# Kernel tuning notes

Hardware: AMD Instinct MI355X
Metric: run time of the kernel (lower is better)

## Reference

```python
import jax, jax.numpy as jnp
import numpy as np
from jax import lax

THRESH = 0.1  # stand-in for os.environ['THRESHOLD']
DN = ('NCHW', 'OIHW', 'NCHW')


def _prelu(x, a):
    # nn.PReLU() with a single shared parameter a (init 0.25)
    return jnp.where(x >= 0, x, a[0] * x)


def _nan_conv(x, w, b):
    # NaNConv2d: skip (zero out) input activations with |x| < THRESH,
    # then a standard 3x3 conv, stride 1, padding 1.
    xm = jnp.where(jnp.abs(x) >= THRESH, x, jnp.zeros((), x.dtype))
    y = lax.conv_general_dilated(xm, w, window_strides=(1, 1),
                                 padding='SAME', dimension_numbers=DN)
    return y + b[None, :, None, None]


def setup_inputs() -> dict:
    key = jax.random.key(0)
    ks = jax.random.split(key, 8)
    B, C, H, W = 8, 256, 128, 128
    x = jax.random.normal(ks[0], (B, C, H, W), dtype=jnp.float32)
    w_scale = 0.05  # keep activations numerically tame
    w1 = jax.random.normal(ks[1], (C, C, 3, 3), dtype=jnp.float32) * w_scale
    b1 = jax.random.normal(ks[2], (C,), dtype=jnp.float32) * w_scale
    w2 = jax.random.normal(ks[3], (C, C, 3, 3), dtype=jnp.float32) * w_scale
    b2 = jax.random.normal(ks[4], (C,), dtype=jnp.float32) * w_scale
    w3 = jax.random.normal(ks[5], (C, C, 3, 3), dtype=jnp.float32) * w_scale
    b3 = jax.random.normal(ks[6], (C,), dtype=jnp.float32) * w_scale
    prelu_a = jnp.full((1,), 0.25, dtype=jnp.float32)  # nn.PReLU default init
    return {'x': x, 'w1': w1, 'b1': b1, 'w2': w2, 'b2': b2,
            'w3': w3, 'b3': b3, 'prelu_a': prelu_a}


def reference(x, w1, b1, w2, b2, w3, b3, prelu_a):
    # x0 = NaNConv(prelu(x))
    x0 = _nan_conv(_prelu(x, prelu_a), w1, b1)
    # cat+max over trailing dim == elementwise max
    x1_max = jnp.maximum(x, x0)
    x1 = _prelu(x1_max, prelu_a)
    x1c = _nan_conv(x1, w2, b2)
    x2_max = jnp.maximum(x1c, x1_max)
    x2 = _prelu(x2_max, prelu_a)
    out = _nan_conv(x2, w3, b3)
    return out
```

## Files before the change

### kernel.cpp

```cpp
#include <hip/hip_runtime.h>
#include <cstddef>

#define THRESH 0.1f

constexpr int Bn = 8, C = 256, H = 128, W = 128;
constexpr int HW = H * W;
constexpr size_t CHW = (size_t)C * HW;
constexpr int WSZ = 9 * 256 * 256;
constexpr int WT_ELEM = 18432;
constexpr int ACT_ELEM = 4 * 132 * 32;
constexpr int SA_BYTES = (WT_ELEM + ACT_ELEM) * 2;

typedef __attribute__((ext_vector_type(8))) short short8;
typedef __attribute__((ext_vector_type(4))) float f32x4;

__device__ __forceinline__ float bf2f(ushort u) {
    union { unsigned u; float f; } v; v.u = ((unsigned)u) << 16; return v.f;
}
__device__ __forceinline__ ushort f2bf(float f) {
    union { float f; unsigned u; } v; v.f = f;
    unsigned r = v.u + 0x7FFF + ((v.u >> 16) & 1);
    return (ushort)(r >> 16);
}
__device__ __forceinline__ float pm(float x, float a) {
    float t = (x >= 0.f) ? x : a * x;
    return (fabsf(t) >= THRESH) ? t : 0.f;
}

__device__ __forceinline__ void load_lds16(const void* g, void* l) {
    __builtin_amdgcn_global_load_lds(
        (const __attribute__((address_space(1))) unsigned int*)g,
        (__attribute__((address_space(3))) unsigned int*)l, 16, 0, 0);
}

__global__ void wtrans_kernel(const float* __restrict__ w1,
                              const float* __restrict__ w2,
                              const float* __restrict__ w3,
                              ushort* __restrict__ Wtf)
{
    const float* src = (blockIdx.z == 0) ? w1 : (blockIdx.z == 1) ? w2 : w3;
    ushort* dst = Wtf + (size_t)blockIdx.z * WSZ;
    int idx = blockIdx.x * 256 + threadIdx.x;
    int co = idx >> 8, ci = idx & 255;
    int cb  = co >> 6;
    int m   = (co >> 4) & 3;
    int l15 = co & 15;
    int cib = ci >> 5;
    int l4  = (ci >> 3) & 3;
    int j   = ci & 7;
    int lane = l15 + 16 * l4;
    for (int t = 0; t < 9; ++t) {
        float v = src[((size_t)co * 256 + ci) * 9 + t];
        size_t o = ((((size_t)cb * 8 + cib) * 9 + t) * 4 + m) * 512 + lane * 8 + j;
        dst[o] = f2bf(v);
    }
}

__global__ __launch_bounds__(256) void xt1_kernel(const float* __restrict__ x,
                                                  const float* __restrict__ pa,
                                                  ushort* __restrict__ Xt)
{
    __shared__ float sl[64][133];
    int tid = threadIdx.x;
    int ci0 = blockIdx.x * 64, h = blockIdx.y, b = blockIdx.z;
    float a = pa[0];
    int wcol = tid & 127, chalf = tid >> 7;
    const float* xb = x + (size_t)b * CHW + (size_t)ci0 * HW + h * W;
    for (int r = 0; r < 32; ++r) {
        int ci = r * 2 + chalf;
        sl[ci][wcol] = pm(xb[(size_t)ci * HW + wcol], a);
    }
    __syncthreads();
    ushort* dst = Xt + ((size_t)(b * H + h)) * W * C + ci0;
    for (int r = 0; r < 4; ++r) {
        int c = r * 256 + tid;
        int wc = c >> 3, cic = c & 7;
        unsigned p0 = f2bf(sl[cic*8+0][wc]) | ((unsigned)f2bf(sl[cic*8+1][wc]) << 16);
        unsigned p1 = f2bf(sl[cic*8+2][wc]) | ((unsigned)f2bf(sl[cic*8+3][wc]) << 16);
        unsigned p2 = f2bf(sl[cic*8+4][wc]) | ((unsigned)f2bf(sl[cic*8+5][wc]) << 16);
        unsigned p3 = f2bf(sl[cic*8+6][wc]) | ((unsigned)f2bf(sl[cic*8+7][wc]) << 16);
        uint4 v = {p0, p1, p2, p3};
        *(uint4*)(dst + (size_t)wc * C + cic * 8) = v;
    }
}

template <int MODE>
__global__ __launch_bounds__(256, 2) void conv_kernel(
    const ushort* __restrict__ Xt, const ushort* __restrict__ Wtf,
    const float* __restrict__ bias, const float* __restrict__ pa,
    const float* __restrict__ xf,
    ushort* __restrict__ xmax,
    ushort* __restrict__ XtOut,
    float* __restrict__ out)
{
    extern __shared__ __align__(16) ushort sa[];
    ushort* sw = sa;
    ushort* sact = sa + WT_ELEM;

    const int tid = threadIdx.x, lane = tid & 63, wv = tid >> 6;
    const int orig = blockIdx.x;
    const int vid = (orig & 7) * 256 + (orig >> 3);
    const int cb = vid & 3, by = vid >> 2;
    const int co0 = cb * 64;
    const int b = by >> 6, h0 = (by & 63) * 2;
    const int l15 = lane & 15, l4 = lane >> 4;
    const int hrow = wv >> 1, whalf = wv & 1;

    {
        uint4 z = {0, 0, 0, 0};
        uint4* zp = (uint4*)sact;
        for (int i = tid; i < ACT_ELEM / 8; i += 256) zp[i] = z;
    }

    f32x4 acc[4][4];
    const f32x4 z4 = {0.f, 0.f, 0.f, 0.f};
#pragma unroll
    for (int m = 0; m < 4; ++m)
#pragma unroll
        for (int n = 0; n < 4; ++n) acc[m][n] = z4;

    const ushort* xb = Xt + (size_t)b * H * W * C;
    const int sr = wv;
    const int shh = h0 - 1 + sr;
    const bool svalid = (unsigned)shh < 128u;
    const ushort* sgbase = xb + (size_t)shh * W * C;
    const int lchunk = lane >> 2, lsub = lane & 3;

    for (int cib = 0; cib < 8; ++cib) {
        const int ci0 = cib * 32;
        __syncthreads();
        {
            const ushort* wsrc = Wtf + ((size_t)cb * 8 + cib) * WT_ELEM;
#pragma unroll
            for (int g = 0; g < 9; ++g) {
                int ch = wv * 576 + g * 64;
                load_lds16(wsrc + (size_t)(ch + lane) * 8, sw + (size_t)ch * 8);
            }
        }
        if (svalid) {
#pragma unroll
            for (int seg = 0; seg < 8; ++seg) {
                int ww = seg * 16 + lchunk;
                int key = ((sr * 132 + 1 + ww) >> 1) & 3;
                const void* gp = sgbase + (size_t)ww * C + ci0 + ((lsub ^ key) << 3);
                load_lds16(gp, sact + (sr * 132 + 1) * 32 + seg * 512);
            }
        }
        __syncthreads();

#pragma unroll
        for (int ky = 0; ky < 3; ++ky) {
            const int r = hrow + ky;
#pragma unroll
            for (int kx = 0; kx < 3; ++kx) {
                const int t = ky * 3 + kx;
                short8 af[4], bfv[4];
#pragma unroll
                for (int m = 0; m < 4; ++m)
                    af[m] = *(const short8*)(sw + (size_t)(t * 4 + m) * 512 + lane * 8);
#pragma unroll
                for (int n = 0; n < 4; ++n) {
                    int wi = whalf * 64 + n * 16 + l15 + kx;
                    int row = r * 132 + wi;
                    int key = (row >> 1) & 3;
                    bfv[n] = *(const short8*)(sact + row * 32 + ((l4 ^ key) << 3));
                }
#pragma unroll
                for (int m = 0; m < 4; ++m)
#pragma unroll
                    for (int n = 0; n < 4; ++n)
                        acc[m][n] = __builtin_amdgcn_mfma_f32_16x16x32_bf16(
                            af[m], bfv[n], acc[m][n], 0, 0, 0);
            }
        }
    }

    const int h = h0 + hrow;
    const float ap = (MODE != 0) ? pa[0] : 0.f;
#pragma unroll
    for (int m = 0; m < 4; ++m) {
        const int cobase = co0 + m * 16 + l4 * 4;
        const f32x4 bv = *(const f32x4*)(bias + cobase);
#pragma unroll
        for (int n = 0; n < 4; ++n) {
            const int wc = whalf * 64 + n * 16 + l15;
            if constexpr (MODE == 0) {
#pragma unroll
                for (int rr = 0; rr < 4; ++rr)
                    out[((size_t)(b * C + cobase + rr) * H + h) * W + wc] =
                        acc[m][n][rr] + bv[rr];
            } else {
                const size_t nb = ((size_t)(b * H + h) * W + wc) * C + cobase;
                float mm[4];
                if constexpr (MODE == 1) {
#pragma unroll
                    for (int rr = 0; rr < 4; ++rr) {
                        float vv = acc[m][n][rr] + bv[rr];
                        float xv = xf[((size_t)(b * C + cobase + rr) * H + h) * W + wc];
                        mm[rr] = fmaxf(xv, vv);
                    }
                    uint2 um = {(unsigned)f2bf(mm[0]) | ((unsigned)f2bf(mm[1]) << 16),
                                (unsigned)f2bf(mm[2]) | ((unsigned)f2bf(mm[3]) << 16)};
                    *(uint2*)(xmax + nb) = um;
                } else {
                    uint2 mv = *(const uint2*)(xmax + nb);
                    mm[0] = fmaxf(acc[m][n][0] + bv[0], bf2f((ushort)(mv.x & 0xffffu)));
                    mm[1] = fmaxf(acc[m][n][1] + bv[1], bf2f((ushort)(mv.x >> 16)));
                    mm[2] = fmaxf(acc[m][n][2] + bv[2], bf2f((ushort)(mv.y & 0xffffu)));
                    mm[3] = fmaxf(acc[m][n][3] + bv[3], bf2f((ushort)(mv.y >> 16)));
                }
                uint2 px = {(unsigned)f2bf(pm(mm[0], ap)) | ((unsigned)f2bf(pm(mm[1], ap)) << 16),
                            (unsigned)f2bf(pm(mm[2], ap)) | ((unsigned)f2bf(pm(mm[3], ap)) << 16)};
                *(uint2*)(XtOut + nb) = px;
            }
        }
    }
}

extern "C" void kernel_launch(void* const* d_in, const int* in_sizes, int n_in,
                              void* d_out, int out_size, void* d_ws, size_t ws_size,
                              hipStream_t stream)
{
    const float* x  = (const float*)d_in[0];
    const float* w1 = (const float*)d_in[1];
    const float* b1 = (const float*)d_in[2];
    const float* w2 = (const float*)d_in[3];
    const float* b2 = (const float*)d_in[4];
    const float* w3 = (const float*)d_in[5];
    const float* b3 = (const float*)d_in[6];
    const float* pa = (const float*)d_in[7];

    char* ws = (char*)d_ws;
    ushort* Xt1  = (ushort*)ws;
    ushort* Xt2  = (ushort*)(ws + 67108864);
    ushort* xmax = (ushort*)(ws + 134217728);
    ushort* Wtf  = (ushort*)(ws + 201326592);

    static bool attr_done = false;
    if (!attr_done) {
        hipFuncSetAttribute((const void*)conv_kernel<0>,
                            hipFuncAttributeMaxDynamicSharedMemorySize, SA_BYTES);
        hipFuncSetAttribute((const void*)conv_kernel<1>,
                            hipFuncAttributeMaxDynamicSharedMemorySize, SA_BYTES);
        hipFuncSetAttribute((const void*)conv_kernel<2>,
                            hipFuncAttributeMaxDynamicSharedMemorySize, SA_BYTES);
        attr_done = true;
    }

    dim3 tg(4, 128, 8), tb(256);

    wtrans_kernel<<<dim3(256, 1, 3), 256, 0, stream>>>(w1, w2, w3, Wtf);
    xt1_kernel<<<tg, tb, 0, stream>>>(x, pa, Xt1);
    conv_kernel<1><<<dim3(2048), tb, SA_BYTES, stream>>>(Xt1, Wtf, b1, pa, x, xmax, Xt2, nullptr);
    conv_kernel<2><<<dim3(2048), tb, SA_BYTES, stream>>>(Xt2, Wtf + WSZ, b2, pa, nullptr, xmax, Xt1, nullptr);
    conv_kernel<0><<<dim3(2048), tb, SA_BYTES, stream>>>(Xt1, Wtf + 2 * WSZ, b3, pa, nullptr, nullptr, nullptr, (float*)d_out);
}
```

Baseline: 667.5 us.

## Process four output rows per block to reuse staged weights across two row pairs

Each block now computes two row pairs (four rows) per 64-channel tile, keeping two accumulator sets, so each staged weight slice in shared memory serves twice as much output. The grid halves to 1024 blocks. This is meant to halve weight reloads from global memory, at the cost of doubled accumulator registers (risking spills or lower occupancy under launch bounds of 2), extra barriers for restaging activations, and fewer blocks for load balance.

Measured after the change: 674.0 us. Within noise of the previous version (+1.0%).

```diff
diff --git a/kernel.cpp b/kernel.cpp
--- a/kernel.cpp
+++ b/kernel.cpp
@@ -99,10 +99,10 @@
 
     const int tid = threadIdx.x, lane = tid & 63, wv = tid >> 6;
     const int orig = blockIdx.x;
-    const int vid = (orig & 7) * 256 + (orig >> 3);
-    const int cb = vid & 3, by = vid >> 2;
+    const int vid = (orig & 7) * 128 + (orig >> 3);
+    const int cb = vid & 3, byq = vid >> 2;
     const int co0 = cb * 64;
-    const int b = by >> 6, h0 = (by & 63) * 2;
+    const int b = byq >> 5, h0 = (byq & 31) * 4;
     const int l15 = lane & 15, l4 = lane >> 4;
     const int hrow = wv >> 1, whalf = wv & 1;
 
@@ -112,42 +112,39 @@
         for (int i = tid; i < ACT_ELEM / 8; i += 256) zp[i] = z;
     }
 
-    f32x4 acc[4][4];
+    f32x4 acc0[4][4], acc1[4][4];
     const f32x4 z4 = {0.f, 0.f, 0.f, 0.f};
 #pragma unroll
     for (int m = 0; m < 4; ++m)
 #pragma unroll
-        for (int n = 0; n < 4; ++n) acc[m][n] = z4;
+        for (int n = 0; n < 4; ++n) { acc0[m][n] = z4; acc1[m][n] = z4; }
 
     const ushort* xb = Xt + (size_t)b * H * W * C;
     const int sr = wv;
-    const int shh = h0 - 1 + sr;
-    const bool svalid = (unsigned)shh < 128u;
-    const ushort* sgbase = xb + (size_t)shh * W * C;
     const int lchunk = lane >> 2, lsub = lane & 3;
 
-    for (int cib = 0; cib < 8; ++cib) {
-        const int ci0 = cib * 32;
-        __syncthreads();
-        {
-            const ushort* wsrc = Wtf + ((size_t)cb * 8 + cib) * WT_ELEM;
-#pragma unroll
-            for (int g = 0; g < 9; ++g) {
-                int ch = wv * 576 + g * 64;
-                load_lds16(wsrc + (size_t)(ch + lane) * 8, sw + (size_t)ch * 8);
-            }
-        }
-        if (svalid) {
+    auto stage_acts = [&](int hp, int cib) {
+        const int shh = h0 + 2 * hp - 1 + sr;
+        ushort* slb = sact + (sr * 132 + 1) * 32;
+        if ((unsigned)shh < 128u) {
+            const ushort* sgbase = xb + (size_t)shh * W * C;
+            const int ci0 = cib * 32;
 #pragma unroll
             for (int seg = 0; seg < 8; ++seg) {
                 int ww = seg * 16 + lchunk;
                 int key = ((sr * 132 + 1 + ww) >> 1) & 3;
                 const void* gp = sgbase + (size_t)ww * C + ci0 + ((lsub ^ key) << 3);
-                load_lds16(gp, sact + (sr * 132 + 1) * 32 + seg * 512);
-            }
-        }
-        __syncthreads();
-
+                load_lds16(gp, slb + seg * 512);
+            }
+        } else {
+            uint4 z = {0, 0, 0, 0};
+#pragma unroll
+            for (int seg = 0; seg < 8; ++seg)
+                *(uint4*)(slb + seg * 512 + lane * 8) = z;
+        }
+    };
+
+    auto compute = [&](f32x4 (&acc)[4][4]) {
 #pragma unroll
         for (int ky = 0; ky < 3; ++ky) {
             const int r = hrow + ky;
@@ -173,45 +170,69 @@
                             af[m], bfv[n], acc[m][n], 0, 0, 0);
             }
         }
-    }
-
-    const int h = h0 + hrow;
+    };
+
+    for (int cib = 0; cib < 8; ++cib) {
+        __syncthreads();
+        {
+            const ushort* wsrc = Wtf + ((size_t)cb * 8 + cib) * WT_ELEM;
+#pragma unroll
+            for (int g = 0; g < 9; ++g) {
+                int ch = wv * 576 + g * 64;
+                load_lds16(wsrc + (size_t)(ch + lane) * 8, sw + (size_t)ch * 8);
+            }
+        }
+        stage_acts(0, cib);
+        __syncthreads();
+        compute(acc0);
+
+        __syncthreads();
+        stage_acts(1, cib);
+        __syncthreads();
+        compute(acc1);
+    }
+
     const float ap = (MODE != 0) ? pa[0] : 0.f;
 #pragma unroll
-    for (int m = 0; m < 4; ++m) {
-        const int cobase = co0 + m * 16 + l4 * 4;
-        const f32x4 bv = *(const f32x4*)(bias + cobase);
-#pragma unroll
-        for (int n = 0; n < 4; ++n) {
-            const int wc = whalf * 64 + n * 16 + l15;
-            if constexpr (MODE == 0) {
-#pragma unroll
-                for (int rr = 0; rr < 4; ++rr)
-                    out[((size_t)(b * C + cobase + rr) * H + h) * W + wc] =
-                        acc[m][n][rr] + bv[rr];
-            } else {
-                const size_t nb = ((size_t)(b * H + h) * W + wc) * C + cobase;
-                float mm[4];
-                if constexpr (MODE == 1) {
-#pragma unroll
-                    for (int rr = 0; rr < 4; ++rr) {
-                        float vv = acc[m][n][rr] + bv[rr];
-                        float xv = xf[((size_t)(b * C + cobase + rr) * H + h) * W + wc];
-                        mm[rr] = fmaxf(xv, vv);
+    for (int hp = 0; hp < 2; ++hp) {
+        const f32x4 (&acc)[4][4] = hp ? acc1 : acc0;
+        const int h = h0 + 2 * hp + hrow;
+#pragma unroll
+        for (int m = 0; m < 4; ++m) {
+            const int cobase = co0 + m * 16 + l4 * 4;
+            const f32x4 bv = *(const f32x4*)(bias + cobase);
+#pragma unroll
+            for (int n = 0; n < 4; ++n) {
+                const int wc = whalf * 64 + n * 16 + l15;
+                if constexpr (MODE == 0) {
+#pragma unroll
+                    for (int rr = 0; rr < 4; ++rr)
+                        out[((size_t)(b * C + cobase + rr) * H + h) * W + wc] =
+                            acc[m][n][rr] + bv[rr];
+                } else {
+                    const size_t nb = ((size_t)(b * H + h) * W + wc) * C + cobase;
+                    float mm[4];
+                    if constexpr (MODE == 1) {
+#pragma unroll
+                        for (int rr = 0; rr < 4; ++rr) {
+                            float vv = acc[m][n][rr] + bv[rr];
+                            float xv = xf[((size_t)(b * C + cobase + rr) * H + h) * W + wc];
+                            mm[rr] = fmaxf(xv, vv);
+                        }
+                        uint2 um = {(unsigned)f2bf(mm[0]) | ((unsigned)f2bf(mm[1]) << 16),
+                                    (unsigned)f2bf(mm[2]) | ((unsigned)f2bf(mm[3]) << 16)};
+                        *(uint2*)(xmax + nb) = um;
+                    } else {
+                        uint2 mv = *(const uint2*)(xmax + nb);
+                        mm[0] = fmaxf(acc[m][n][0] + bv[0], bf2f((ushort)(mv.x & 0xffffu)));
+                        mm[1] = fmaxf(acc[m][n][1] + bv[1], bf2f((ushort)(mv.x >> 16)));
+                        mm[2] = fmaxf(acc[m][n][2] + bv[2], bf2f((ushort)(mv.y & 0xffffu)));
+                        mm[3] = fmaxf(acc[m][n][3] + bv[3], bf2f((ushort)(mv.y >> 16)));
                     }
-                    uint2 um = {(unsigned)f2bf(mm[0]) | ((unsigned)f2bf(mm[1]) << 16),
-                                (unsigned)f2bf(mm[2]) | ((unsigned)f2bf(mm[3]) << 16)};
-                    *(uint2*)(xmax + nb) = um;
-                } else {
-                    uint2 mv = *(const uint2*)(xmax + nb);
-                    mm[0] = fmaxf(acc[m][n][0] + bv[0], bf2f((ushort)(mv.x & 0xffffu)));
-                    mm[1] = fmaxf(acc[m][n][1] + bv[1], bf2f((ushort)(mv.x >> 16)));
-                    mm[2] = fmaxf(acc[m][n][2] + bv[2], bf2f((ushort)(mv.y & 0xffffu)));
-                    mm[3] = fmaxf(acc[m][n][3] + bv[3], bf2f((ushort)(mv.y >> 16)));
+                    uint2 px = {(unsigned)f2bf(pm(mm[0], ap)) | ((unsigned)f2bf(pm(mm[1], ap)) << 16),
+                                (unsigned)f2bf(pm(mm[2], ap)) | ((unsigned)f2bf(pm(mm[3], ap)) << 16)};
+                    *(uint2*)(XtOut + nb) = px;
                 }
-                uint2 px = {(unsigned)f2bf(pm(mm[0], ap)) | ((unsigned)f2bf(pm(mm[1], ap)) << 16),
-                            (unsigned)f2bf(pm(mm[2], ap)) | ((unsigned)f2bf(pm(mm[3], ap)) << 16)};
-                *(uint2*)(XtOut + nb) = px;
             }
         }
     }
@@ -251,7 +272,7 @@
 
     wtrans_kernel<<<dim3(256, 1, 3), 256, 0, stream>>>(w1, w2, w3, Wtf);
     xt1_kernel<<<tg, tb, 0, stream>>>(x, pa, Xt1);
-    conv_kernel<1><<<dim3(2048), tb, SA_BYTES, stream>>>(Xt1, Wtf, b1, pa, x, xmax, Xt2, nullptr);
-    conv_kernel<2><<<dim3(2048), tb, SA_BYTES, stream>>>(Xt2, Wtf + WSZ, b2, pa, nullptr, xmax, Xt1, nullptr);
-    conv_kernel<0><<<dim3(2048), tb, SA_BYTES, stream>>>(Xt1, Wtf + 2 * WSZ, b3, pa, nullptr, nullptr, nullptr, (float*)d_out);
-}
+    conv_kernel<1><<<dim3(1024), tb, SA_BYTES, stream>>>(Xt1, Wtf, b1, pa, x, xmax, Xt2, nullptr);
+    conv_kernel<2><<<dim3(1024), tb, SA_BYTES, stream>>>(Xt2, Wtf + WSZ, b2, pa, nullptr, xmax, Xt1, nullptr);
+    conv_kernel<0><<<dim3(1024), tb, SA_BYTES, stream>>>(Xt1, Wtf + 2 * WSZ, b3, pa, nullptr, nullptr, nullptr, (float*)d_out);
+}
```
